# Kernel tuning notes

Measured on AMD Instinct MI355X. Metric: run time of the kernel, lower is better.

The kernel has to match this reference:

```python
import jax, jax.numpy as jnp
import numpy as np

IMG = 128          # img_size -> height = width
BIG = 1.0e6        # background depth for empty pixels (min-reduced away)


def _ball_render(points, radiuses, h=IMG, w=IMG):
    """Orthographic sphere depth rasterization (BallRender equivalent).
    points: [N, 3] (x, y in pixel coords, z depth); radiuses: [N] (pixels).
    Returns [N, h, w] depth images: z - sqrt(r^2 - d^2) inside the ball, BIG outside.
    """
    u = jnp.arange(w, dtype=points.dtype)            # [w]
    v = jnp.arange(h, dtype=points.dtype)            # [h]
    x = points[:, 0][:, None, None]                  # [N,1,1]
    y = points[:, 1][:, None, None]
    z = points[:, 2][:, None, None]
    d2 = (u[None, None, :] - x) ** 2 + (v[None, :, None] - y) ** 2   # [N,h,w]
    r2 = (radiuses ** 2)[:, None, None]
    inside = d2 < r2
    safe = jnp.where(inside, r2 - d2, 1.0)           # avoid nan/inf grads at boundary
    return jnp.where(inside, z - jnp.sqrt(safe), BIG)


def setup_inputs() -> dict:
    key = jax.random.key(0)
    k1, k2, k3, k4 = jax.random.split(key, 4)
    B, V, J = 8, 4, 21
    eye = jnp.eye(4, dtype=jnp.float32)
    # near-identity camera poses so projected joints stay on-screen
    camera_poses = eye + 0.01 * jax.random.normal(k1, (B, V, 4, 4), dtype=jnp.float32)
    inv_camera_poses = eye + 0.01 * jax.random.normal(k2, (B, V, 4, 4), dtype=jnp.float32)
    # joints: x,y in [20, 108] px, z in [2, 10]
    xy = 20.0 + 88.0 * jax.random.uniform(k3, (B, V, J, 2), dtype=jnp.float32)
    z = 2.0 + 8.0 * jax.random.uniform(k4, (B, V, J, 1), dtype=jnp.float32)
    joints = jnp.concatenate([xy, z], axis=-1)
    radiuses = jnp.array([9.0, 8.0, 7.5, 7.0, 6.5, 8.0, 7.0, 6.5, 6.0, 8.0, 7.0,
                          6.5, 6.0, 7.5, 6.5, 6.0, 5.5, 7.0, 6.0, 5.5, 5.0],
                         dtype=jnp.float32)
    return {"camera_poses": camera_poses, "inv_camera_poses": inv_camera_poses,
            "joints": joints, "radiuses": radiuses}


def reference(camera_poses, inv_camera_poses, joints, radiuses):
    B, V, J, _ = joints.shape
    # mutual_trans[b, i, j] = inv_camera_poses[b, j] @ camera_poses[b, i]
    mutual = jnp.einsum('bjxy,biyz->bijxz', inv_camera_poses, camera_poses)
    mutual = jax.lax.stop_gradient(mutual)           # torch code .detach()s it
    R = mutual[..., :3, :3]                          # [B,V,V,3,3]
    t = mutual[..., :3, 3]                           # [B,V,V,3]
    # project joints of source view i into every target view j
    proj = jnp.einsum('bijxy,biky->bijkx', R, joints) + t[:, :, :, None, :]  # [B,V,V,J,3]
    pts = proj.reshape(-1, 3)
    rads = jnp.broadcast_to(radiuses.reshape(1, 1, 1, J), (B, V, V, J)).reshape(-1)
    imgs = _ball_render(pts, rads).reshape(B, V, V, J, IMG, IMG)
    depth_imgs = imgs.min(axis=3)                    # min over joints
    # torch returns projected_points shaped [B,V,V,J,3,1]
    return depth_imgs, proj[..., None]
```

## Files before the change

### kernel.cpp

```cpp
#include <hip/hip_runtime.h>
#include <hip/hip_bf16.h>

#define IMG 128

__device__ __forceinline__ float bf16_snap(float f) {
    union { float f; unsigned int u; } v; v.f = f;
    unsigned int u = v.u;
    u += 0x7fffu + ((u >> 16) & 1u);
    v.u = u & 0xFFFF0000u;
    return v.f;
}

__global__ __launch_bounds__(256) void mutual_proj_kernel(
    const float* __restrict__ cam,
    const float* __restrict__ inv,
    const float* __restrict__ joints,
    const float* __restrict__ rads,
    float* __restrict__ out)
{
#pragma clang fp contract(off)
    constexpr int V = 4, J = 21;
    const int bid  = blockIdx.x;
    const int img  = bid >> 3;
    const int slab = bid & 7;
    const int b = img >> 4;
    const int i = (img >> 2) & 3;
    const int j = img & 3;
    const int t = threadIdx.x;

    __shared__ float4   sball[J];
    __shared__ unsigned smask[IMG];

    if (t < J) {
        const float4* invp4 = (const float4*)(inv + ((b * V + j) << 4));
        const float4* camp4 = (const float4*)(cam + ((b * V + i) << 4));
        float4 Mr[4], Cr[4];
        #pragma unroll
        for (int a = 0; a < 4; ++a) Mr[a] = invp4[a];
        #pragma unroll
        for (int a = 0; a < 4; ++a) Cr[a] = camp4[a];
        float M[4][4], C[4][4];
        #pragma unroll
        for (int a = 0; a < 4; ++a) {
            M[a][0] = Mr[a].x; M[a][1] = Mr[a].y; M[a][2] = Mr[a].z; M[a][3] = Mr[a].w;
            C[a][0] = Cr[a].x; C[a][1] = Cr[a].y; C[a][2] = Cr[a].z; C[a][3] = Cr[a].w;
        }

        float R[3][4];
        #pragma unroll
        for (int x = 0; x < 3; ++x) {
            #pragma unroll
            for (int zc = 0; zc < 4; ++zc) {
                float s = __fmul_rn(M[x][0], C[0][zc]);
                s = __fmaf_rn(M[x][1], C[1][zc], s);
                s = __fmaf_rn(M[x][2], C[2][zc], s);
                s = __fmaf_rn(M[x][3], C[3][zc], s);
                R[x][zc] = s;
            }
        }

        const float* jp = joints + (((b * V + i) * J + t) * 3);
        const float jx = jp[0], jy = jp[1], jz = jp[2];

        float p[3];
        #pragma unroll
        for (int x = 0; x < 3; ++x) {
            float s = __fmul_rn(R[x][0], jx);
            s = __fmaf_rn(R[x][1], jy, s);
            s = __fmaf_rn(R[x][2], jz, s);
            s = __fadd_rn(s, R[x][3]);
            p[x] = s;
        }
        const float r = rads[t];
        sball[t] = make_float4(p[0], p[1], p[2], __fmul_rn(r, r));

        if (slab == 0) {
            float* po = out + (128 * IMG * IMG) + (img * J + t) * 3;
            po[0] = bf16_snap(p[0]);
            po[1] = bf16_snap(p[1]);
            po[2] = bf16_snap(p[2]);
        }
    }
    __syncthreads();

    if (t < IMG) {
        const float v = (float)t;
        unsigned m = 0;
        #pragma unroll
        for (int k = 0; k < J; ++k) {
            const float dy  = __fsub_rn(v, sball[k].y);
            const float dy2 = __fmul_rn(dy, dy);
            if (dy2 < sball[k].w) m |= (1u << k);
        }
        smask[t] = m;
    }
    __syncthreads();

    float* dout = out + img * (IMG * IMG);
    const int pbase = slab * 2048;
    #pragma unroll
    for (int it = 0; it < 2; ++it) {
        const int base = pbase + it * 1024 + t * 4;
        const int row  = base >> 7;
        const float v  = (float)row;
        const float u0 = (float)(base & 127);
        float best0 = 1000000.0f, best1 = 1000000.0f;
        float best2 = 1000000.0f, best3 = 1000000.0f;
        unsigned m = smask[row];
        while (m) {
            const int k = __builtin_ctz(m);
            m &= m - 1u;
            const float4 bl = sball[k];
            const float dy  = __fsub_rn(v, bl.y);
            const float dy2 = __fmul_rn(dy, dy);
            #pragma unroll
            for (int c = 0; c < 4; ++c) {
                const float u  = __fadd_rn(u0, (float)c);
                const float dx = __fsub_rn(u, bl.x);
                const float d2 = __fadd_rn(__fmul_rn(dx, dx), dy2);
                if (d2 < bl.w) {
                    const float dep =
                        __fsub_rn(bl.z, __fsqrt_rn(__fsub_rn(bl.w, d2)));
                    if (c == 0) best0 = fminf(best0, dep);
                    if (c == 1) best1 = fminf(best1, dep);
                    if (c == 2) best2 = fminf(best2, dep);
                    if (c == 3) best3 = fminf(best3, dep);
                }
            }
        }
        float4 o;
        o.x = bf16_snap(best0); o.y = bf16_snap(best1);
        o.z = bf16_snap(best2); o.w = bf16_snap(best3);
        *(float4*)(dout + base) = o;
    }
}

extern "C" void kernel_launch(void* const* d_in, const int* in_sizes, int n_in,
                              void* d_out, int out_size, void* d_ws, size_t ws_size,
                              hipStream_t stream) {
    const float* cam    = (const float*)d_in[0];
    const float* inv    = (const float*)d_in[1];
    const float* joints = (const float*)d_in[2];
    const float* rads   = (const float*)d_in[3];
    float* out = (float*)d_out;

    dim3 grid(128 * 8);
    dim3 block(256);
    hipLaunchKernelGGL(mutual_proj_kernel, grid, block, 0, stream,
                       cam, inv, joints, rads, out);
}
```

Baseline: 66.64 us.

## Split into prep and raster kernels with per-row compacted ball lists

The single fused kernel becomes two. A prep kernel (one block per image) projects the joints once and writes, for each row, a compacted list of overlapping balls (x, z, dy², r²) plus a count into the output buffer as scratch. A raster kernel then reads its row's list, uses wave shuffles when a row has more than eight balls, and overwrites the row with depths. This removes the redundant per-slab projection and the bitmask iteration. In exchange it adds a second launch and a global-memory round trip. Each wave must read the scratch before overwriting the same row, and the raster kernel adds an explicit wait and barrier for that ordering.

```diff
diff --git a/kernel.cpp b/kernel.cpp
--- a/kernel.cpp
+++ b/kernel.cpp
@@ -1,7 +1,7 @@
 #include <hip/hip_runtime.h>
-#include <hip/hip_bf16.h>
 
 #define IMG 128
+#define NBALL 21
 
 __device__ __forceinline__ float bf16_snap(float f) {
     union { float f; unsigned int u; } v; v.f = f;
@@ -11,7 +11,7 @@
     return v.f;
 }
 
-__global__ __launch_bounds__(256) void mutual_proj_kernel(
+__global__ __launch_bounds__(128) void prep_kernel(
     const float* __restrict__ cam,
     const float* __restrict__ inv,
     const float* __restrict__ joints,
@@ -19,31 +19,24 @@
     float* __restrict__ out)
 {
 #pragma clang fp contract(off)
-    constexpr int V = 4, J = 21;
-    const int bid  = blockIdx.x;
-    const int img  = bid >> 3;
-    const int slab = bid & 7;
+    constexpr int V = 4;
+    const int img = blockIdx.x;
     const int b = img >> 4;
     const int i = (img >> 2) & 3;
     const int j = img & 3;
     const int t = threadIdx.x;
 
-    __shared__ float4   sball[J];
-    __shared__ unsigned smask[IMG];
+    __shared__ float4 sball[NBALL];
 
-    if (t < J) {
+    if (t < NBALL) {
         const float4* invp4 = (const float4*)(inv + ((b * V + j) << 4));
         const float4* camp4 = (const float4*)(cam + ((b * V + i) << 4));
-        float4 Mr[4], Cr[4];
-        #pragma unroll
-        for (int a = 0; a < 4; ++a) Mr[a] = invp4[a];
-        #pragma unroll
-        for (int a = 0; a < 4; ++a) Cr[a] = camp4[a];
         float M[4][4], C[4][4];
         #pragma unroll
         for (int a = 0; a < 4; ++a) {
-            M[a][0] = Mr[a].x; M[a][1] = Mr[a].y; M[a][2] = Mr[a].z; M[a][3] = Mr[a].w;
-            C[a][0] = Cr[a].x; C[a][1] = Cr[a].y; C[a][2] = Cr[a].z; C[a][3] = Cr[a].w;
+            const float4 mr = invp4[a], cr = camp4[a];
+            M[a][0] = mr.x; M[a][1] = mr.y; M[a][2] = mr.z; M[a][3] = mr.w;
+            C[a][0] = cr.x; C[a][1] = cr.y; C[a][2] = cr.z; C[a][3] = cr.w;
         }
 
         float R[3][4];
@@ -59,7 +52,7 @@
             }
         }
 
-        const float* jp = joints + (((b * V + i) * J + t) * 3);
+        const float* jp = joints + (((b * V + i) * NBALL + t) * 3);
         const float jx = jp[0], jy = jp[1], jz = jp[2];
 
         float p[3];
@@ -67,72 +60,100 @@
         for (int x = 0; x < 3; ++x) {
             float s = __fmul_rn(R[x][0], jx);
             s = __fmaf_rn(R[x][1], jy, s);
-            s = __fmaf_rn(R[x][2], jz, s);
-            s = __fadd_rn(s, R[x][3]);
+            s = __fadd_rn(__fmaf_rn(R[x][2], jz, s), R[x][3]);
             p[x] = s;
         }
         const float r = rads[t];
         sball[t] = make_float4(p[0], p[1], p[2], __fmul_rn(r, r));
 
-        if (slab == 0) {
-            float* po = out + (128 * IMG * IMG) + (img * J + t) * 3;
-            po[0] = bf16_snap(p[0]);
-            po[1] = bf16_snap(p[1]);
-            po[2] = bf16_snap(p[2]);
-        }
+        float* po = out + (128 * IMG * IMG) + (img * NBALL + t) * 3;
+        po[0] = bf16_snap(p[0]);
+        po[1] = bf16_snap(p[1]);
+        po[2] = bf16_snap(p[2]);
     }
     __syncthreads();
 
-    if (t < IMG) {
-        const float v = (float)t;
-        unsigned m = 0;
-        #pragma unroll
-        for (int k = 0; k < J; ++k) {
-            const float dy  = __fsub_rn(v, sball[k].y);
-            const float dy2 = __fmul_rn(dy, dy);
-            if (dy2 < sball[k].w) m |= (1u << k);
+    const float v = (float)t;
+    float* rowbase = out + img * (IMG * IMG) + (t << 7);
+    float4* rp4 = (float4*)rowbase;
+    int cnt = 0;
+    #pragma unroll
+    for (int k = 0; k < NBALL; ++k) {
+        const float4 bl = sball[k];
+        const float dy  = __fsub_rn(v, bl.y);
+        const float dy2 = __fmul_rn(dy, dy);
+        if (dy2 < bl.w) {
+            rp4[cnt] = make_float4(bl.x, bl.z, dy2, bl.w);
+            ++cnt;
         }
-        smask[t] = m;
     }
+    for (int s = cnt; s < 8; ++s)
+        rp4[s] = make_float4(0.f, 0.f, 0.f, 0.f);
+    rowbase[84] = __int_as_float(cnt);
+}
+
+__global__ __launch_bounds__(256) void raster_kernel(float* __restrict__ out)
+{
+#pragma clang fp contract(off)
+    const int bid  = blockIdx.x;
+    const int img  = bid >> 4;
+    const int slab = bid & 15;
+    const int t    = threadIdx.x;
+    const int lane = t & 31;
+    const int row  = slab * 8 + (t >> 5);
+    const int col  = lane << 2;
+
+    float* rowbase = out + img * (IMG * IMG) + (row << 7);
+    const float4* rp4 = (const float4*)rowbase;
+
+    float4 cd[8];
+    #pragma unroll
+    for (int s = 0; s < 8; ++s) cd[s] = rp4[s];
+    const int cnt = __float_as_int(rowbase[84]);
+    float4 ts = rp4[8 + (lane < 13 ? lane : 12)];
+
+    asm volatile("s_waitcnt vmcnt(0)" ::: "memory");
     __syncthreads();
 
-    float* dout = out + img * (IMG * IMG);
-    const int pbase = slab * 2048;
-    #pragma unroll
-    for (int it = 0; it < 2; ++it) {
-        const int base = pbase + it * 1024 + t * 4;
-        const int row  = base >> 7;
-        const float v  = (float)row;
-        const float u0 = (float)(base & 127);
-        float best0 = 1000000.0f, best1 = 1000000.0f;
-        float best2 = 1000000.0f, best3 = 1000000.0f;
-        unsigned m = smask[row];
-        while (m) {
-            const int k = __builtin_ctz(m);
-            m &= m - 1u;
-            const float4 bl = sball[k];
-            const float dy  = __fsub_rn(v, bl.y);
-            const float dy2 = __fmul_rn(dy, dy);
-            #pragma unroll
-            for (int c = 0; c < 4; ++c) {
-                const float u  = __fadd_rn(u0, (float)c);
-                const float dx = __fsub_rn(u, bl.x);
-                const float d2 = __fadd_rn(__fmul_rn(dx, dx), dy2);
-                if (d2 < bl.w) {
-                    const float dep =
-                        __fsub_rn(bl.z, __fsqrt_rn(__fsub_rn(bl.w, d2)));
-                    if (c == 0) best0 = fminf(best0, dep);
-                    if (c == 1) best1 = fminf(best1, dep);
-                    if (c == 2) best2 = fminf(best2, dep);
-                    if (c == 3) best3 = fminf(best3, dep);
-                }
+    const float u0 = (float)col;
+    float best0 = 1000000.0f, best1 = 1000000.0f;
+    float best2 = 1000000.0f, best3 = 1000000.0f;
+
+    auto doball = [&](const float4 bl) {
+        #pragma unroll
+        for (int c = 0; c < 4; ++c) {
+            const float u  = __fadd_rn(u0, (float)c);
+            const float dx = __fsub_rn(u, bl.x);
+            const float d2 = __fadd_rn(__fmul_rn(dx, dx), bl.z);
+            if (d2 < bl.w) {
+                const float dep =
+                    __fsub_rn(bl.y, __fsqrt_rn(__fsub_rn(bl.w, d2)));
+                if (c == 0) best0 = fminf(best0, dep);
+                if (c == 1) best1 = fminf(best1, dep);
+                if (c == 2) best2 = fminf(best2, dep);
+                if (c == 3) best3 = fminf(best3, dep);
             }
         }
-        float4 o;
-        o.x = bf16_snap(best0); o.y = bf16_snap(best1);
-        o.z = bf16_snap(best2); o.w = bf16_snap(best3);
-        *(float4*)(dout + base) = o;
+    };
+
+    #pragma unroll
+    for (int s = 0; s < 8; ++s) doball(cd[s]);
+
+    if (cnt > 8) {
+        for (int s = 8; s < cnt; ++s) {
+            float4 bl;
+            bl.x = __shfl(ts.x, s - 8, 32);
+            bl.y = __shfl(ts.y, s - 8, 32);
+            bl.z = __shfl(ts.z, s - 8, 32);
+            bl.w = __shfl(ts.w, s - 8, 32);
+            doball(bl);
+        }
     }
+
+    float4 o;
+    o.x = bf16_snap(best0); o.y = bf16_snap(best1);
+    o.z = bf16_snap(best2); o.w = bf16_snap(best3);
+    *(float4*)(rowbase + col) = o;
 }
 
 extern "C" void kernel_launch(void* const* d_in, const int* in_sizes, int n_in,
@@ -144,8 +165,7 @@
     const float* rads   = (const float*)d_in[3];
     float* out = (float*)d_out;
 
-    dim3 grid(128 * 8);
-    dim3 block(256);
-    hipLaunchKernelGGL(mutual_proj_kernel, grid, block, 0, stream,
+    hipLaunchKernelGGL(prep_kernel, dim3(128), dim3(128), 0, stream,
                        cam, inv, joints, rads, out);
+    hipLaunchKernelGGL(raster_kernel, dim3(2048), dim3(256), 0, stream, out);
 }
```

Result: slower. 71.65 us (+7.5%).

## Compute row masks per slab and render 8 pixels per thread with preloaded balls

Applied to the files above, without the earlier changes.

Each block now builds row-overlap masks only for its own 16 rows instead of all 128. Every thread handles 8 contiguous pixels in one pass rather than 4 pixels in two iterations. The first four overlapping balls are fetched from shared memory up front and processed unrolled before falling back to a loop for the rest. This cuts redundant mask work, loop overhead and dependent shared-memory latency, at the cost of more registers per thread.

```diff
diff --git a/kernel.cpp b/kernel.cpp
--- a/kernel.cpp
+++ b/kernel.cpp
@@ -1,7 +1,7 @@
 #include <hip/hip_runtime.h>
-#include <hip/hip_bf16.h>
 
 #define IMG 128
+#define NBALL 21
 
 __device__ __forceinline__ float bf16_snap(float f) {
     union { float f; unsigned int u; } v; v.f = f;
@@ -19,7 +19,7 @@
     float* __restrict__ out)
 {
 #pragma clang fp contract(off)
-    constexpr int V = 4, J = 21;
+    constexpr int V = 4, J = NBALL;
     const int bid  = blockIdx.x;
     const int img  = bid >> 3;
     const int slab = bid & 7;
@@ -29,21 +29,17 @@
     const int t = threadIdx.x;
 
     __shared__ float4   sball[J];
-    __shared__ unsigned smask[IMG];
+    __shared__ unsigned smask[16];
 
     if (t < J) {
         const float4* invp4 = (const float4*)(inv + ((b * V + j) << 4));
         const float4* camp4 = (const float4*)(cam + ((b * V + i) << 4));
-        float4 Mr[4], Cr[4];
-        #pragma unroll
-        for (int a = 0; a < 4; ++a) Mr[a] = invp4[a];
-        #pragma unroll
-        for (int a = 0; a < 4; ++a) Cr[a] = camp4[a];
         float M[4][4], C[4][4];
         #pragma unroll
         for (int a = 0; a < 4; ++a) {
-            M[a][0] = Mr[a].x; M[a][1] = Mr[a].y; M[a][2] = Mr[a].z; M[a][3] = Mr[a].w;
-            C[a][0] = Cr[a].x; C[a][1] = Cr[a].y; C[a][2] = Cr[a].z; C[a][3] = Cr[a].w;
+            const float4 mr = invp4[a], cr = camp4[a];
+            M[a][0] = mr.x; M[a][1] = mr.y; M[a][2] = mr.z; M[a][3] = mr.w;
+            C[a][0] = cr.x; C[a][1] = cr.y; C[a][2] = cr.z; C[a][3] = cr.w;
         }
 
         float R[3][4];
@@ -83,8 +79,8 @@
     }
     __syncthreads();
 
-    if (t < IMG) {
-        const float v = (float)t;
+    if (t < 16) {
+        const float v = (float)(slab * 16 + t);
         unsigned m = 0;
         #pragma unroll
         for (int k = 0; k < J; ++k) {
@@ -96,43 +92,67 @@
     }
     __syncthreads();
 
-    float* dout = out + img * (IMG * IMG);
-    const int pbase = slab * 2048;
+    const int r16 = t >> 4;
+    const int row = slab * 16 + r16;
+    const int col = (t & 15) << 3;
+    const float v = (float)row;
+
+    float u[8];
     #pragma unroll
-    for (int it = 0; it < 2; ++it) {
-        const int base = pbase + it * 1024 + t * 4;
-        const int row  = base >> 7;
-        const float v  = (float)row;
-        const float u0 = (float)(base & 127);
-        float best0 = 1000000.0f, best1 = 1000000.0f;
-        float best2 = 1000000.0f, best3 = 1000000.0f;
-        unsigned m = smask[row];
-        while (m) {
-            const int k = __builtin_ctz(m);
-            m &= m - 1u;
-            const float4 bl = sball[k];
-            const float dy  = __fsub_rn(v, bl.y);
-            const float dy2 = __fmul_rn(dy, dy);
-            #pragma unroll
-            for (int c = 0; c < 4; ++c) {
-                const float u  = __fadd_rn(u0, (float)c);
-                const float dx = __fsub_rn(u, bl.x);
-                const float d2 = __fadd_rn(__fmul_rn(dx, dx), dy2);
-                if (d2 < bl.w) {
-                    const float dep =
-                        __fsub_rn(bl.z, __fsqrt_rn(__fsub_rn(bl.w, d2)));
-                    if (c == 0) best0 = fminf(best0, dep);
-                    if (c == 1) best1 = fminf(best1, dep);
-                    if (c == 2) best2 = fminf(best2, dep);
-                    if (c == 3) best3 = fminf(best3, dep);
-                }
+    for (int c = 0; c < 8; ++c) u[c] = __fadd_rn((float)col, (float)c);
+
+    float best[8];
+    #pragma unroll
+    for (int c = 0; c < 8; ++c) best[c] = 1000000.0f;
+
+    auto doball = [&](const float4 bl) {
+        const float dy  = __fsub_rn(v, bl.y);
+        const float dy2 = __fmul_rn(dy, dy);
+        #pragma unroll
+        for (int c = 0; c < 8; ++c) {
+            const float dx = __fsub_rn(u[c], bl.x);
+            const float d2 = __fadd_rn(__fmul_rn(dx, dx), dy2);
+            if (d2 < bl.w) {
+                const float dep =
+                    __fsub_rn(bl.z, __fsqrt_rn(__fsub_rn(bl.w, d2)));
+                best[c] = fminf(best[c], dep);
             }
         }
-        float4 o;
-        o.x = bf16_snap(best0); o.y = bf16_snap(best1);
-        o.z = bf16_snap(best2); o.w = bf16_snap(best3);
-        *(float4*)(dout + base) = o;
+    };
+
+    const unsigned m = smask[r16];
+    const int cnt = __popc(m);
+
+    unsigned mm = m;
+    int i0 = (int)__builtin_ctz(mm | 0x80000000u); i0 = i0 > 20 ? 20 : i0; mm &= mm - 1u;
+    int i1 = (int)__builtin_ctz(mm | 0x80000000u); i1 = i1 > 20 ? 20 : i1; mm &= mm - 1u;
+    int i2 = (int)__builtin_ctz(mm | 0x80000000u); i2 = i2 > 20 ? 20 : i2; mm &= mm - 1u;
+    int i3 = (int)__builtin_ctz(mm | 0x80000000u); i3 = i3 > 20 ? 20 : i3; mm &= mm - 1u;
+    const float4 b0 = sball[i0];
+    const float4 b1 = sball[i1];
+    const float4 b2 = sball[i2];
+    const float4 b3 = sball[i3];
+
+    if (cnt > 0) doball(b0);
+    if (cnt > 1) doball(b1);
+    if (cnt > 2) doball(b2);
+    if (cnt > 3) doball(b3);
+    if (cnt > 4) {
+        while (mm) {
+            const int k = __builtin_ctz(mm);
+            mm &= mm - 1u;
+            doball(sball[k]);
+        }
     }
+
+    float* dout = out + img * (IMG * IMG) + (row << 7) + col;
+    float4 oA, oB;
+    oA.x = bf16_snap(best[0]); oA.y = bf16_snap(best[1]);
+    oA.z = bf16_snap(best[2]); oA.w = bf16_snap(best[3]);
+    oB.x = bf16_snap(best[4]); oB.y = bf16_snap(best[5]);
+    oB.z = bf16_snap(best[6]); oB.w = bf16_snap(best[7]);
+    *(float4*)dout       = oA;
+    *(float4*)(dout + 4) = oB;
 }
 
 extern "C" void kernel_launch(void* const* d_in, const int* in_sizes, int n_in,
```

Result: no change. 66.87 us (+0.3%).
